# Performance work log

Hardware: AMD Instinct MI355X
Metric: run time of the kernel (lower is better)

Reference implementation:

```python
import jax, jax.numpy as jnp
import numpy as np

B, S, DIM, HID, E, TOPK = 32, 512, 1024, 4096, 8, 2
CF = 1.0


def setup_inputs() -> dict:
    key = jax.random.key(0)
    ks = jax.random.split(key, 12)
    sc = 0.02
    return {
        "router_input": jax.random.normal(ks[0], (B, S, DIM), jnp.float32),
        "x": jax.random.normal(ks[1], (B, S, DIM), jnp.float32),
        "noise": jax.random.normal(ks[2], (B, E), jnp.float32),
        # router params (stored [in,out])
        "Wg": jax.random.normal(ks[3], (DIM, E), jnp.float32) * sc,
        "bg": jnp.zeros((E,), jnp.float32),
        "Wn": jax.random.normal(ks[4], (DIM, E), jnp.float32) * sc,
        "bn": jnp.zeros((E,), jnp.float32),
        # expert MLP params, stacked over experts
        "W1": jax.random.normal(ks[5], (E, DIM, HID), jnp.float32) * sc,
        "b1": jnp.zeros((E, HID), jnp.float32),
        "W2": jax.random.normal(ks[6], (E, HID, DIM), jnp.float32) * sc,
        "b2": jnp.zeros((E, DIM), jnp.float32),
    }


def reference(router_input, x, noise, Wg, bg, Wn, bn, W1, b1, W2, b2):
    b, s, d = x.shape
    e = Wg.shape[1]
    # ---- noisy top-k router (per-sample: mean over sequence) ----
    ri = router_input.mean(axis=1)                      # [B, D]
    logits = ri @ Wg + bg                               # [B, E]
    noise_logits = ri @ Wn + bn                         # [B, E]
    noisy = logits + noise * jax.nn.softplus(noise_logits)
    top_vals, top_idx = jax.lax.top_k(noisy, TOPK)      # [B, K]
    # softmax over -inf-masked logits == softmax over the kept top-k values
    gate = jax.nn.softmax(top_vals, axis=-1)            # [B, K]

    flat_e = top_idx.reshape(-1)                        # [N] expert id per (sample,k) pair
    flat_w = gate.reshape(-1)                           # [N]
    sample_ids = jnp.repeat(jnp.arange(b), TOPK)        # [N]
    n = b * TOPK
    capacity = max(int(n / e * CF), 1)

    # ---- capacity drop: keep first `capacity` pairs per expert in sorted order ----
    order = jnp.argsort(flat_e, stable=True)            # stable sort by expert id
    sorted_e = flat_e[order]
    rank_in_expert = jnp.arange(n) - jnp.searchsorted(sorted_e, sorted_e, side="left")
    keep = jnp.zeros((n,), bool).at[order].set(rank_in_expert < capacity)

    # ---- per-pair expert MLP via gathered expert weights (grouped GEMM) ----
    xp = x[sample_ids]                                  # [N, S, D]
    h = jnp.einsum("psd,pdh->psh", xp, W1[flat_e]) + b1[flat_e][:, None, :]
    h = jax.nn.gelu(h, approximate=False)               # exact GELU (torch nn.GELU)
    y = jnp.einsum("psh,phd->psd", h, W2[flat_e]) + b2[flat_e][:, None, :]

    # ---- weight by gate, zero dropped pairs, combine back per sample ----
    y = y * (flat_w * keep.astype(y.dtype))[:, None, None]
    return jax.ops.segment_sum(y, sample_ids, num_segments=b)  # [B, S, D]
```

## Files before the change

kernel.cpp:

```cpp
#include <hip/hip_runtime.h>
#include <hip/hip_bf16.h>
#include <math.h>

#define B_    32
#define S_    512
#define DIM_  1024
#define HID_  4096
#define E_    8
#define TOPK_ 2
#define CAP_  8
#define NSLOT_ 64

typedef __bf16 bf16_t;
typedef bf16_t bf16x8 __attribute__((ext_vector_type(8)));
typedef float  f32x4  __attribute__((ext_vector_type(4)));

__device__ __forceinline__ ushort f2bf(float f) {
    union { float f; unsigned u; } v; v.f = f;
    unsigned r = (v.u + 0x7fffu + ((v.u >> 16) & 1u)) >> 16;
    return (ushort)r;
}

__device__ __forceinline__ void async_cp16(const ushort* g, ushort* l) {
    __builtin_amdgcn_global_load_lds(
        (const __attribute__((address_space(1))) unsigned int*)g,
        (__attribute__((address_space(3))) unsigned int*)l, 16, 0, 0);
}

__global__ void k_mean_p(const float* __restrict__ rin, float* __restrict__ part) {
    int p = blockIdx.x, b = blockIdx.y;
    int d4 = threadIdx.x;
    const float4* base = (const float4*)(rin + ((size_t)b * S_ + p * 32) * DIM_) + d4;
    float4 acc = {0.f, 0.f, 0.f, 0.f};
    for (int s = 0; s < 32; ++s) {
        float4 v = base[(size_t)s * (DIM_ / 4)];
        acc.x += v.x; acc.y += v.y; acc.z += v.z; acc.w += v.w;
    }
    ((float4*)(part + (size_t)(b * 16 + p) * DIM_))[d4] = acc;
}

__global__ void k_mean_f(const float* __restrict__ part, float* __restrict__ ri) {
    int b = blockIdx.x, d4 = threadIdx.x;
    float4 acc = {0.f, 0.f, 0.f, 0.f};
    for (int p = 0; p < 16; ++p) {
        float4 v = ((const float4*)(part + (size_t)(b * 16 + p) * DIM_))[d4];
        acc.x += v.x; acc.y += v.y; acc.z += v.z; acc.w += v.w;
    }
    const float inv = 1.0f / (float)S_;
    float4 o = {acc.x * inv, acc.y * inv, acc.z * inv, acc.w * inv};
    ((float4*)(ri + (size_t)b * DIM_))[d4] = o;
}

__global__ void k_router_logits(const float* __restrict__ ri, const float* __restrict__ noise,
                                const float* __restrict__ Wg, const float* __restrict__ bg,
                                const float* __restrict__ Wn, const float* __restrict__ bn,
                                float* __restrict__ noisy) {
    __shared__ float rrow[DIM_];
    __shared__ float pg[256], pn[256];
    int b = blockIdx.x, t = threadIdx.x;
    ((float4*)rrow)[t] = ((const float4*)(ri + (size_t)b * DIM_))[t];
    __syncthreads();
    int e = t & 7, c = t >> 3;
    float ag = 0.f, an = 0.f;
    for (int i = 0; i < 32; ++i) {
        float rv = rrow[c * 32 + i];
        ag += rv * Wg[(c * 32 + i) * E_ + e];
        an += rv * Wn[(c * 32 + i) * E_ + e];
    }
    pg[t] = ag; pn[t] = an;
    __syncthreads();
    for (int off = 128; off >= 8; off >>= 1) {
        if (t < off) { pg[t] += pg[t + off]; pn[t] += pn[t + off]; }
        __syncthreads();
    }
    if (t < E_) {
        float lg = pg[t] + bg[t];
        float ln = pn[t] + bn[t];
        float sp = (ln > 20.f) ? ln : log1pf(expf(ln));
        noisy[b * E_ + t] = lg + noise[b * E_ + t] * sp;
    }
}

__global__ void k_router_assign(const float* __restrict__ noisy,
                                int* __restrict__ slot_sample, float* __restrict__ slot_gate,
                                int* __restrict__ sample_slot, float* __restrict__ sample_gate) {
    __shared__ int   top_i[B_][TOPK_];
    __shared__ float top_g[B_][TOPK_];
    int t = threadIdx.x;
    if (t < B_) {
        float v1 = -INFINITY, v2 = -INFINITY; int i1 = 0, i2 = 0;
        for (int ee = 0; ee < E_; ++ee) {
            float v = noisy[t * E_ + ee];
            if (v > v1)      { v2 = v1; i2 = i1; v1 = v; i1 = ee; }
            else if (v > v2) { v2 = v; i2 = ee; }
        }
        float g2 = expf(v2 - v1);
        float s = 1.f + g2;
        top_i[t][0] = i1; top_i[t][1] = i2;
        top_g[t][0] = 1.f / s; top_g[t][1] = g2 / s;
    }
    if (t < NSLOT_)      { slot_sample[t] = -1; slot_gate[t] = 0.f; }
    if (t < B_ * TOPK_)  { sample_slot[t] = -1; sample_gate[t] = 0.f; }
    __syncthreads();
    if (t == 0) {
        int cnt[E_];
        for (int ee = 0; ee < E_; ++ee) cnt[ee] = 0;
        for (int p = 0; p < B_ * TOPK_; ++p) {
            int bb = p >> 1, kk = p & 1;
            int ee = top_i[bb][kk];
            int c = cnt[ee]++;
            if (c < CAP_) {
                int slot = ee * CAP_ + c;
                slot_sample[slot] = bb;
                slot_gate[slot]   = top_g[bb][kk];
                sample_slot[bb * TOPK_ + kk] = slot;
                sample_gate[bb * TOPK_ + kk] = top_g[bb][kk];
            }
        }
    }
}

__global__ void k_cvt_x(const float* __restrict__ x, ushort* __restrict__ xb, int n8) {
    int i = blockIdx.x * blockDim.x + threadIdx.x;
    if (i >= n8) return;
    const float4* p = (const float4*)x + (size_t)i * 2;
    float4 a = p[0], b = p[1];
    union { ushort s[8]; uint4 v; } u;
    u.s[0] = f2bf(a.x); u.s[1] = f2bf(a.y); u.s[2] = f2bf(a.z); u.s[3] = f2bf(a.w);
    u.s[4] = f2bf(b.x); u.s[5] = f2bf(b.y); u.s[6] = f2bf(b.z); u.s[7] = f2bf(b.w);
    ((uint4*)xb)[i] = u.v;
}

__global__ void k_transpose_cvt(const float* __restrict__ W, ushort* __restrict__ Wt,
                                int K, int N) {
    __shared__ float tile[64][65];
    size_t eoff = (size_t)blockIdx.z * K * N;
    const float* Win = W + eoff;
    ushort* Wout = Wt + eoff;
    int n0 = blockIdx.x * 64, k0 = blockIdx.y * 64;
    int t = threadIdx.x;
    int r = t >> 4;
    int c4 = (t & 15) << 2;
#pragma unroll
    for (int i = 0; i < 4; ++i) {
        float4 v = *(const float4*)(Win + (size_t)(k0 + r + i * 16) * N + n0 + c4);
        tile[r + i * 16][c4 + 0] = v.x;
        tile[r + i * 16][c4 + 1] = v.y;
        tile[r + i * 16][c4 + 2] = v.z;
        tile[r + i * 16][c4 + 3] = v.w;
    }
    __syncthreads();
#pragma unroll
    for (int i = 0; i < 4; ++i) {
        int nn = r + i * 16;
        ushort4 o;
        o.x = f2bf(tile[c4 + 0][nn]);
        o.y = f2bf(tile[c4 + 1][nn]);
        o.z = f2bf(tile[c4 + 2][nn]);
        o.w = f2bf(tile[c4 + 3][nn]);
        *(ushort4*)(Wout + (size_t)(n0 + nn) * K + k0 + c4) = o;
    }
}

__device__ __forceinline__ void gemm_mainloop256(
    const ushort* __restrict__ Abase, int lda,
    const ushort* __restrict__ Bbase, int ldb,
    int K, ushort* lds, f32x4 acc[8][4]) {
    const int tid  = threadIdx.x;
    const int wave = tid >> 6, lane = tid & 63;
    const int wm = wave >> 2, wn = wave & 3;
    const int quad = lane >> 4, mr = lane & 15;
    const int nt = K >> 5;
    const unsigned swz = (((unsigned)(mr & 3)) << 4) | (((unsigned)((mr >> 2) & 1)) << 6);
    unsigned offA[8], offB[4];
#pragma unroll
    for (int i = 0; i < 8; ++i)
        offA[i] = (((unsigned)(wm * 128 + i * 16 + mr) * 64u + (unsigned)quad * 16u) ^ swz);
#pragma unroll
    for (int j = 0; j < 4; ++j)
        offB[j] = 16384u + (((unsigned)(wn * 64 + j * 16 + mr) * 64u + (unsigned)quad * 16u) ^ swz);
    int srow[2], squad[2];
    unsigned sldso[2];
#pragma unroll
    for (int h = 0; h < 2; ++h) {
        unsigned tt = (unsigned)(2 * wave + h) * 1024u + (unsigned)lane * 16u;
        int row = (int)(((tt >> 7) << 1) | (((tt >> 6) & 1u) ^ ((tt >> 8) & 1u)));
        int q   = (int)(((tt >> 4) & 3u) ^ (unsigned)(row & 3));
        srow[h] = row; squad[h] = q;
        sldso[h] = (unsigned)(2 * wave + h) * 1024u;
    }
    const ushort* gA0 = Abase + (size_t)srow[0] * lda + squad[0] * 8;
    const ushort* gA1 = Abase + (size_t)srow[1] * lda + squad[1] * 8;
    const ushort* gB0 = Bbase + (size_t)srow[0] * ldb + squad[0] * 8;
    const ushort* gB1 = Bbase + (size_t)srow[1] * ldb + squad[1] * 8;
    char* ldsb = (char*)lds;
#define STAGE_A_(tt_) do { \
        char* s_ = ldsb + ((tt_) & 3) * 32768; int k0_ = (tt_) * 32; \
        async_cp16(gA0 + k0_, (ushort*)(s_ + sldso[0])); \
        async_cp16(gA1 + k0_, (ushort*)(s_ + sldso[1])); } while (0)
#define STAGE_B_(tt_) do { \
        char* s_ = ldsb + ((tt_) & 3) * 32768 + 16384; int k0_ = (tt_) * 32; \
        async_cp16(gB0 + k0_, (ushort*)(s_ + sldso[0])); \
        async_cp16(gB1 + k0_, (ushort*)(s_ + sldso[1])); } while (0)
    STAGE_A_(0); STAGE_B_(0); STAGE_A_(1); STAGE_B_(1);
    asm volatile("s_waitcnt vmcnt(4)" ::: "memory");
    __builtin_amdgcn_s_barrier();
    for (int t = 0; t < nt; ++t) {
        const char* sb = ldsb + (t & 3) * 32768;
        bf16x8 a[4], b[4];
#pragma unroll
        for (int i = 0; i < 4; ++i) a[i] = *(const bf16x8*)(sb + offA[i]);
#pragma unroll
        for (int j = 0; j < 4; ++j) b[j] = *(const bf16x8*)(sb + offB[j]);
        if (t + 2 < nt) STAGE_A_(t + 2);
        __builtin_amdgcn_s_barrier();
        asm volatile("s_waitcnt lgkmcnt(0)" ::: "memory");
        __builtin_amdgcn_sched_barrier(0);
        __builtin_amdgcn_s_setprio(1);
#pragma unroll
        for (int i = 0; i < 4; ++i)
#pragma unroll
            for (int j = 0; j < 4; ++j)
                acc[i][j] = __builtin_amdgcn_mfma_f32_16x16x32_bf16(a[i], b[j], acc[i][j], 0, 0, 0);
        __builtin_amdgcn_s_setprio(0);
        __builtin_amdgcn_s_barrier();
#pragma unroll
        for (int i = 0; i < 4; ++i) a[i] = *(const bf16x8*)(sb + offA[4 + i]);
        if (t + 2 < nt) STAGE_B_(t + 2);
        __builtin_amdgcn_s_barrier();
        asm volatile("s_waitcnt lgkmcnt(0)" ::: "memory");
        __builtin_amdgcn_sched_barrier(0);
        __builtin_amdgcn_s_setprio(1);
#pragma unroll
        for (int i = 0; i < 4; ++i)
#pragma unroll
            for (int j = 0; j < 4; ++j)
                acc[4 + i][j] = __builtin_amdgcn_mfma_f32_16x16x32_bf16(a[i], b[j], acc[4 + i][j], 0, 0, 0);
        __builtin_amdgcn_s_setprio(0);
        if (t + 2 < nt)      { asm volatile("s_waitcnt vmcnt(4)" ::: "memory"); }
        else if (t + 1 < nt) { asm volatile("s_waitcnt vmcnt(0)" ::: "memory"); }
        __builtin_amdgcn_s_barrier();
    }
#undef STAGE_A_
#undef STAGE_B_
}

__global__ __launch_bounds__(512, 2) void k_gemm1(
    const ushort* __restrict__ xb, const ushort* __restrict__ w1t,
    const float* __restrict__ b1, const int* __restrict__ slot_sample,
    ushort* __restrict__ H) {
    __shared__ __attribute__((aligned(16))) ushort lds[65536];
    unsigned F = blockIdx.x;
    int low3 = F & 7; unsigned rest = F >> 3;
    int nt_ = rest & 15; int g = rest >> 4;
    int u1 = g * 8 + low3;
    int slot = u1 >> 1, mt = u1 & 1;
    int samp = slot_sample[slot];
    if (samp < 0) return;
    int e = slot >> 3;
    const ushort* Abase = xb + ((size_t)samp * S_ + mt * 256) * DIM_;
    const ushort* Bbase = w1t + (size_t)e * HID_ * DIM_ + (size_t)(nt_ * 256) * DIM_;
    f32x4 acc[8][4];
#pragma unroll
    for (int i = 0; i < 8; ++i)
#pragma unroll
        for (int j = 0; j < 4; ++j) acc[i][j] = (f32x4){0.f, 0.f, 0.f, 0.f};
    gemm_mainloop256(Abase, DIM_, Bbase, DIM_, DIM_, lds, acc);
    int wave = threadIdx.x >> 6, lane = threadIdx.x & 63;
    int wm = wave >> 2, wn = wave & 3, quad = lane >> 4, mr = lane & 15;
    ushort* Hrow = H + ((size_t)slot * S_ + mt * 256) * HID_ + nt_ * 256;
#pragma unroll
    for (int j = 0; j < 4; ++j) {
        int nl = wn * 64 + j * 16 + mr;
        float bias = b1[e * HID_ + nt_ * 256 + nl];
#pragma unroll
        for (int i = 0; i < 8; ++i) {
#pragma unroll
            for (int r = 0; r < 4; ++r) {
                int ml = wm * 128 + i * 16 + quad * 4 + r;
                float v = acc[i][j][r] + bias;
                float gl = 0.5f * v * (1.0f + erff(v * 0.70710678118654752f));
                Hrow[(size_t)ml * HID_ + nl] = f2bf(gl);
            }
        }
    }
}

__global__ __launch_bounds__(512, 2) void k_gemm2(
    const ushort* __restrict__ H, const ushort* __restrict__ w2t,
    const float* __restrict__ b2, const int* __restrict__ sample_slot,
    const float* __restrict__ sample_gate, float* __restrict__ out) {
    __shared__ __attribute__((aligned(16))) ushort lds[65536];
    unsigned F = blockIdx.x;
    int low3 = F & 7; unsigned rest = F >> 3;
    int nt_ = rest & 3; int g = rest >> 2;
    int u = g * 8 + low3;
    int b = u >> 1, mt = u & 1;
    int sl0 = sample_slot[b * TOPK_ + 0], sl1 = sample_slot[b * TOPK_ + 1];
    float ga0 = sample_gate[b * TOPK_ + 0], ga1 = sample_gate[b * TOPK_ + 1];
    if (sl0 < 0) { sl0 = sl1; ga0 = ga1; sl1 = -1; }
    f32x4 acc[8][4];
#pragma unroll
    for (int i = 0; i < 8; ++i)
#pragma unroll
        for (int j = 0; j < 4; ++j) acc[i][j] = (f32x4){0.f, 0.f, 0.f, 0.f};
    if (sl0 >= 0) {
        int e0 = sl0 >> 3;
        gemm_mainloop256(H + ((size_t)sl0 * S_ + mt * 256) * HID_, HID_,
                         w2t + (size_t)e0 * DIM_ * HID_ + (size_t)(nt_ * 256) * HID_, HID_,
                         HID_, lds, acc);
    }
    if (sl1 >= 0) {
        float ratio = ga0 / ga1;
#pragma unroll
        for (int i = 0; i < 8; ++i)
#pragma unroll
            for (int j = 0; j < 4; ++j) acc[i][j] = acc[i][j] * ratio;
        int e1 = sl1 >> 3;
        gemm_mainloop256(H + ((size_t)sl1 * S_ + mt * 256) * HID_, HID_,
                         w2t + (size_t)e1 * DIM_ * HID_ + (size_t)(nt_ * 256) * HID_, HID_,
                         HID_, lds, acc);
    }
    float gfin = (sl1 >= 0) ? ga1 : ((sl0 >= 0) ? ga0 : 0.f);
    int wave = threadIdx.x >> 6, lane = threadIdx.x & 63;
    int wm = wave >> 2, wn = wave & 3, quad = lane >> 4, mr = lane & 15;
    float* Orow = out + ((size_t)b * S_ + mt * 256) * DIM_ + nt_ * 256;
#pragma unroll
    for (int j = 0; j < 4; ++j) {
        int nl = wn * 64 + j * 16 + mr;
        float bias = 0.f;
        if (sl0 >= 0) bias += ga0 * b2[(sl0 >> 3) * DIM_ + nt_ * 256 + nl];
        if (sl1 >= 0) bias += ga1 * b2[(sl1 >> 3) * DIM_ + nt_ * 256 + nl];
#pragma unroll
        for (int i = 0; i < 8; ++i) {
#pragma unroll
            for (int r = 0; r < 4; ++r) {
                int ml = wm * 128 + i * 16 + quad * 4 + r;
                Orow[(size_t)ml * DIM_ + nl] = acc[i][j][r] * gfin + bias;
            }
        }
    }
}

extern "C" void kernel_launch(void* const* d_in, const int* in_sizes, int n_in,
                              void* d_out, int out_size, void* d_ws, size_t ws_size,
                              hipStream_t stream) {
    const float* rin   = (const float*)d_in[0];
    const float* x     = (const float*)d_in[1];
    const float* noise = (const float*)d_in[2];
    const float* Wg    = (const float*)d_in[3];
    const float* bg    = (const float*)d_in[4];
    const float* Wn    = (const float*)d_in[5];
    const float* bn    = (const float*)d_in[6];
    const float* W1    = (const float*)d_in[7];
    const float* b1    = (const float*)d_in[8];
    const float* W2    = (const float*)d_in[9];
    const float* b2    = (const float*)d_in[10];
    float* out = (float*)d_out;

    char* ws = (char*)d_ws;
    float*  ri          = (float*)ws;
    int*    slot_sample = (int*)(ws + 131072);
    float*  slot_gate   = (float*)(ws + 131328);
    int*    sample_slot = (int*)(ws + 131584);
    float*  sample_gate = (float*)(ws + 131840);
    ushort* xb  = (ushort*)(ws + 135168);
    ushort* w1t = (ushort*)(ws + 135168 + 33554432);
    ushort* w2t = (ushort*)(ws + 135168 + 33554432 + 67108864);
    ushort* H   = (ushort*)(ws + 135168 + 33554432 + 2 * 67108864);
    float* part  = (float*)H;
    float* noisy = (float*)((char*)H + 2097152);

    k_mean_p<<<dim3(16, B_), 256, 0, stream>>>(rin, part);
    k_mean_f<<<B_, 256, 0, stream>>>(part, ri);
    k_router_logits<<<B_, 256, 0, stream>>>(ri, noise, Wg, bg, Wn, bn, noisy);
    k_router_assign<<<1, 256, 0, stream>>>(noisy, slot_sample, slot_gate,
                                           sample_slot, sample_gate);
    k_cvt_x<<<(B_ * S_ * DIM_ / 8 + 255) / 256, 256, 0, stream>>>(x, xb, B_ * S_ * DIM_ / 8);
    k_transpose_cvt<<<dim3(HID_ / 64, DIM_ / 64, E_), 256, 0, stream>>>(W1, w1t, DIM_, HID_);
    k_transpose_cvt<<<dim3(DIM_ / 64, HID_ / 64, E_), 256, 0, stream>>>(W2, w2t, HID_, DIM_);
    k_gemm1<<<128 * 16, 512, 0, stream>>>(xb, w1t, b1, slot_sample, H);
    k_gemm2<<<64 * 4, 512, 0, stream>>>(H, w2t, b2, sample_slot, sample_gate, out);
}
```

Baseline: 1.067 ms.

## Restructure GEMM mainloop to 64-wide K tiles with double-buffered four-phase pipeline

Rewrites the shared GEMM mainloop to process K in 64-element steps with a two-stage LDS double buffer instead of 32-element steps with a four-stage ring. Each iteration is split into four phases that interleave A-fragment LDS reads, async global-to-LDS copies for the next tile, and MFMA blocks, with per-phase vmcnt waits. It also changes the LDS swizzle and the copy-address mapping. The aim is fewer barriers per unit of K and better overlap of loads with MFMA work, at the cost of a shallower prefetch depth and delicate hand-tuned waitcnt counts.

```diff
diff --git a/kernel.cpp b/kernel.cpp
--- a/kernel.cpp
+++ b/kernel.cpp
@@ -170,79 +170,73 @@
     const int wave = tid >> 6, lane = tid & 63;
     const int wm = wave >> 2, wn = wave & 3;
     const int quad = lane >> 4, mr = lane & 15;
-    const int nt = K >> 5;
-    const unsigned swz = (((unsigned)(mr & 3)) << 4) | (((unsigned)((mr >> 2) & 1)) << 6);
-    unsigned offA[8], offB[4];
-#pragma unroll
-    for (int i = 0; i < 8; ++i)
-        offA[i] = (((unsigned)(wm * 128 + i * 16 + mr) * 64u + (unsigned)quad * 16u) ^ swz);
-#pragma unroll
-    for (int j = 0; j < 4; ++j)
-        offB[j] = 16384u + (((unsigned)(wn * 64 + j * 16 + mr) * 64u + (unsigned)quad * 16u) ^ swz);
-    int srow[2], squad[2];
-    unsigned sldso[2];
-#pragma unroll
-    for (int h = 0; h < 2; ++h) {
-        unsigned tt = (unsigned)(2 * wave + h) * 1024u + (unsigned)lane * 16u;
-        int row = (int)(((tt >> 7) << 1) | (((tt >> 6) & 1u) ^ ((tt >> 8) & 1u)));
-        int q   = (int)(((tt >> 4) & 3u) ^ (unsigned)(row & 3));
-        srow[h] = row; squad[h] = q;
-        sldso[h] = (unsigned)(2 * wave + h) * 1024u;
-    }
-    const ushort* gA0 = Abase + (size_t)srow[0] * lda + squad[0] * 8;
-    const ushort* gA1 = Abase + (size_t)srow[1] * lda + squad[1] * 8;
-    const ushort* gB0 = Bbase + (size_t)srow[0] * ldb + squad[0] * 8;
-    const ushort* gB1 = Bbase + (size_t)srow[1] * ldb + squad[1] * 8;
-    char* ldsb = (char*)lds;
-#define STAGE_A_(tt_) do { \
-        char* s_ = ldsb + ((tt_) & 3) * 32768; int k0_ = (tt_) * 32; \
-        async_cp16(gA0 + k0_, (ushort*)(s_ + sldso[0])); \
-        async_cp16(gA1 + k0_, (ushort*)(s_ + sldso[1])); } while (0)
-#define STAGE_B_(tt_) do { \
-        char* s_ = ldsb + ((tt_) & 3) * 32768 + 16384; int k0_ = (tt_) * 32; \
-        async_cp16(gB0 + k0_, (ushort*)(s_ + sldso[0])); \
-        async_cp16(gB1 + k0_, (ushort*)(s_ + sldso[1])); } while (0)
-    STAGE_A_(0); STAGE_B_(0); STAGE_A_(1); STAGE_B_(1);
-    asm volatile("s_waitcnt vmcnt(4)" ::: "memory");
+    const int nt = K >> 6;
+    char* const ldsc = (char*)lds;
+    const int swzv = (mr & 7) << 4;
+    const int kp0 = (quad * 16) ^ swzv;
+    const int kp1 = (64 + quad * 16) ^ swzv;
+    const int rowoff = lane >> 3;
+    const int kelem  = ((lane & 7) ^ (lane >> 3)) << 3;
+    const ushort* gA = Abase + (size_t)rowoff * lda + kelem;
+    const ushort* gB = Bbase + (size_t)rowoff * ldb + kelem;
+    const int raq0 = (wave < 4) ? (wave * 8) : (128 + (wave - 4) * 8);
+    const int cb0  = wave * 8;
+    ushort* const ldsA0 = lds;
+    ushort* const ldsB0 = lds + 32768;
+#define SAU(q_, st_, k0_) \
+    async_cp16(gA + (size_t)(raq0 + 32 * (q_)) * lda + (k0_), \
+               ldsA0 + (st_) * 16384 + (raq0 + 32 * (q_)) * 64)
+#define SBH(h_, st_, k0_) do { \
+    async_cp16(gB + (size_t)(cb0 + (h_) * 128) * ldb + (k0_), \
+               ldsB0 + (st_) * 16384 + (h_) * 8192 + wave * 512); \
+    async_cp16(gB + (size_t)(cb0 + (h_) * 128 + 64) * ldb + (k0_), \
+               ldsB0 + (st_) * 16384 + (h_) * 8192 + 4096 + wave * 512); } while (0)
+    SBH(0, 0, 0); SBH(1, 0, 0);
+    SAU(0, 0, 0); SAU(1, 0, 0); SAU(2, 0, 0); SAU(3, 0, 0);
+    asm volatile("s_waitcnt vmcnt(3)" ::: "memory");
     __builtin_amdgcn_s_barrier();
+    bf16x8 a00, a01, a10, a11;
+#define PHASE(q_, STAGES_, VMG_, VMNG_) do { \
+    a00 = *(const bf16x8*)(sa + (2 * (q_)) * 2048 + kp0); \
+    a01 = *(const bf16x8*)(sa + (2 * (q_)) * 2048 + kp1); \
+    a10 = *(const bf16x8*)(sa + (2 * (q_) + 1) * 2048 + kp0); \
+    a11 = *(const bf16x8*)(sa + (2 * (q_) + 1) * 2048 + kp1); \
+    if (g) { STAGES_; } \
+    asm volatile("s_waitcnt lgkmcnt(0)" ::: "memory"); \
+    __builtin_amdgcn_sched_barrier(0); \
+    __builtin_amdgcn_s_setprio(1); \
+    _Pragma("unroll") \
+    for (int j = 0; j < 4; ++j) { \
+        acc[2 * (q_)][j]     = __builtin_amdgcn_mfma_f32_16x16x32_bf16(a00, b0[j], acc[2 * (q_)][j], 0, 0, 0); \
+        acc[2 * (q_)][j]     = __builtin_amdgcn_mfma_f32_16x16x32_bf16(a01, b1[j], acc[2 * (q_)][j], 0, 0, 0); \
+        acc[2 * (q_) + 1][j] = __builtin_amdgcn_mfma_f32_16x16x32_bf16(a10, b0[j], acc[2 * (q_) + 1][j], 0, 0, 0); \
+        acc[2 * (q_) + 1][j] = __builtin_amdgcn_mfma_f32_16x16x32_bf16(a11, b1[j], acc[2 * (q_) + 1][j], 0, 0, 0); \
+    } \
+    __builtin_amdgcn_s_setprio(0); \
+    if (g) { asm volatile("s_waitcnt vmcnt(" #VMG_ ")" ::: "memory"); } \
+    else   { asm volatile("s_waitcnt vmcnt(" #VMNG_ ")" ::: "memory"); } \
+    __builtin_amdgcn_s_barrier(); \
+} while (0)
     for (int t = 0; t < nt; ++t) {
-        const char* sb = ldsb + (t & 3) * 32768;
-        bf16x8 a[4], b[4];
-#pragma unroll
-        for (int i = 0; i < 4; ++i) a[i] = *(const bf16x8*)(sb + offA[i]);
-#pragma unroll
-        for (int j = 0; j < 4; ++j) b[j] = *(const bf16x8*)(sb + offB[j]);
-        if (t + 2 < nt) STAGE_A_(t + 2);
-        __builtin_amdgcn_s_barrier();
-        asm volatile("s_waitcnt lgkmcnt(0)" ::: "memory");
-        __builtin_amdgcn_sched_barrier(0);
-        __builtin_amdgcn_s_setprio(1);
-#pragma unroll
-        for (int i = 0; i < 4; ++i)
-#pragma unroll
-            for (int j = 0; j < 4; ++j)
-                acc[i][j] = __builtin_amdgcn_mfma_f32_16x16x32_bf16(a[i], b[j], acc[i][j], 0, 0, 0);
-        __builtin_amdgcn_s_setprio(0);
-        __builtin_amdgcn_s_barrier();
-#pragma unroll
-        for (int i = 0; i < 4; ++i) a[i] = *(const bf16x8*)(sb + offA[4 + i]);
-        if (t + 2 < nt) STAGE_B_(t + 2);
-        __builtin_amdgcn_s_barrier();
-        asm volatile("s_waitcnt lgkmcnt(0)" ::: "memory");
-        __builtin_amdgcn_sched_barrier(0);
-        __builtin_amdgcn_s_setprio(1);
-#pragma unroll
-        for (int i = 0; i < 4; ++i)
-#pragma unroll
-            for (int j = 0; j < 4; ++j)
-                acc[4 + i][j] = __builtin_amdgcn_mfma_f32_16x16x32_bf16(a[i], b[j], acc[4 + i][j], 0, 0, 0);
-        __builtin_amdgcn_s_setprio(0);
-        if (t + 2 < nt)      { asm volatile("s_waitcnt vmcnt(4)" ::: "memory"); }
-        else if (t + 1 < nt) { asm volatile("s_waitcnt vmcnt(0)" ::: "memory"); }
-        __builtin_amdgcn_s_barrier();
-    }
-#undef STAGE_A_
-#undef STAGE_B_
+        const int sb = t & 1, st = sb ^ 1;
+        const int k1 = (t + 1) << 6;
+        const bool g = (t + 1 < nt);
+        const char* sa  = ldsc + sb * 32768 + (wm * 128 + mr) * 128;
+        const char* sbp = ldsc + 65536 + sb * 32768 + (wn * 64 + mr) * 128;
+        bf16x8 b0[4], b1[4];
+#pragma unroll
+        for (int j = 0; j < 4; ++j) {
+            b0[j] = *(const bf16x8*)(sbp + j * 2048 + kp0);
+            b1[j] = *(const bf16x8*)(sbp + j * 2048 + kp1);
+        }
+        PHASE(0, SBH(0, st, k1), 4, 2);
+        PHASE(1, SBH(1, st, k1), 5, 1);
+        PHASE(2, SAU(0, st, k1); SAU(1, st, k1), 6, 0);
+        PHASE(3, SAU(2, st, k1); SAU(3, st, k1), 3, 0);
+    }
+#undef PHASE
+#undef SAU
+#undef SBH
 }
 
 __global__ __launch_bounds__(512, 2) void k_gemm1(
```

Measured after the change: 992.9 us. 7.0% less time.
